# Optimization experiments

Hardware: AMD Instinct MI355X
Metric: run time of the kernel (lower is better)

Reference implementation:

```python
import jax, jax.numpy as jnp
import numpy as np

D_MODEL = 256   # per-head dim in this module
N_HEAD = 8
B, S = 4, 2048
NEG_INF = -1e9  # large negative in place of -inf for numerical safety


def setup_inputs() -> dict:
    key = jax.random.key(0)
    ks = jax.random.split(key, 8)
    d, h = D_MODEL, N_HEAD
    sc = 1.0 / np.sqrt(d)
    return {
        "Q": jax.random.normal(ks[0], (B, S, d), jnp.float32),
        "mask": jax.random.randint(ks[1], (B, S), 0, 2, jnp.int32),
        "WQ_w": jax.random.normal(ks[2], (h * d, d), jnp.float32) * sc,
        "WQ_b": jnp.zeros((h * d,), jnp.float32),
        "WK_w": jax.random.normal(ks[3], (h * d, d), jnp.float32) * sc,
        "WK_b": jnp.zeros((h * d,), jnp.float32),
        "WV_w": jax.random.normal(ks[4], (h * d, d), jnp.float32) * sc,
        "WV_b": jnp.zeros((h * d,), jnp.float32),
        "WO_w": jax.random.normal(ks[5], (d, h * d), jnp.float32) * sc,
        "WO_b": jnp.zeros((d,), jnp.float32),
        "ln_g": jnp.ones((d,), jnp.float32),
        "ln_b": jnp.zeros((d,), jnp.float32),
    }


def reference(Q, mask, WQ_w, WQ_b, WK_w, WK_b, WV_w, WV_b, WO_w, WO_b, ln_g, ln_b):
    b, s, d = Q.shape
    h = N_HEAD
    # projections (torch Linear: x @ W.T + b), split into heads: [b, h, s, d]
    q = (Q @ WQ_w.T + WQ_b).reshape(b, s, h, d).transpose(0, 2, 1, 3)
    k = (Q @ WK_w.T + WK_b).reshape(b, s, h, d).transpose(0, 2, 1, 3)
    v = (Q @ WV_w.T + WV_b).reshape(b, s, h, d).transpose(0, 2, 1, 3)
    # scaled dot-product scores [b, h, q, k]
    scores = jnp.einsum('bhqd,bhkd->bhqk', q, k) / jnp.sqrt(jnp.asarray(d, Q.dtype))
    key_mask = (mask != 0)[:, None, None, :]  # [b,1,1,k]
    scores = jnp.where(key_mask, scores, NEG_INF)
    alpha = jax.nn.softmax(scores, axis=-1)
    out = jnp.einsum('bhqk,bhkd->bhqd', alpha, v)
    out = out.transpose(0, 2, 1, 3).reshape(b, s, h * d)
    out = out @ WO_w.T + WO_b + Q  # dropout is identity in eval
    # LayerNorm over last dim
    mu = out.mean(-1, keepdims=True)
    var = out.var(-1, keepdims=True)
    return (out - mu) / jnp.sqrt(var + 1e-5) * ln_g + ln_b
```

## Files before the change

kernel.cpp:

```cpp
#include <hip/hip_runtime.h>
#include <cstddef>
#include <cstdint>

#define SQ 2048
#define DH 256
#define NH 8
#define BATCH 4
#define MROWS (BATCH*SQ)
#define HID (NH*DH)

typedef __attribute__((ext_vector_type(8)))  short bf16x8;
typedef __attribute__((ext_vector_type(16))) float f32x16;

typedef __attribute__((address_space(1))) const unsigned char gbuf_t;
typedef __attribute__((address_space(3))) unsigned char lbuf_t;

__device__ __forceinline__ void gl_lds16(const void* g, void* l) {
  __builtin_amdgcn_global_load_lds((gbuf_t*)g, (lbuf_t*)l, 16, 0, 0);
}

__device__ __forceinline__ unsigned short f2bf(float f) {
  unsigned u = __float_as_uint(f);
  unsigned r = (u + 0x7FFFu + ((u >> 16) & 1u)) >> 16;
  return (unsigned short)r;
}
__device__ __forceinline__ unsigned pk2(float a, float b) {
  return (unsigned)f2bf(a) | ((unsigned)f2bf(b) << 16);
}
__device__ __forceinline__ float fexp2(float x) {
  float r;
  asm("v_exp_f32 %0, %1" : "=v"(r) : "v"(x));
  return r;
}
__device__ __forceinline__ f32x16 zero16() {
  f32x16 v;
#pragma unroll
  for (int i = 0; i < 16; ++i) v[i] = 0.0f;
  return v;
}

__global__ void __launch_bounds__(256) cvt_kernel(
    const float* __restrict__ X,  const float* __restrict__ Wq,
    const float* __restrict__ Wk, const float* __restrict__ Wv,
    const float* __restrict__ Wo,
    unsigned short* __restrict__ Xb,  unsigned short* __restrict__ Wqb,
    unsigned short* __restrict__ Wkb, unsigned short* __restrict__ Wvb,
    unsigned short* __restrict__ Wob)
{
  int bid = blockIdx.x;
  const float* src; unsigned short* dst; size_t off;
  if      (bid < 512) { src = X;  dst = Xb;  off = (size_t)bid * 4096; }
  else if (bid < 640) { src = Wq; dst = Wqb; off = (size_t)(bid - 512) * 4096; }
  else if (bid < 768) { src = Wk; dst = Wkb; off = (size_t)(bid - 640) * 4096; }
  else if (bid < 896) { src = Wv; dst = Wvb; off = (size_t)(bid - 768) * 4096; }
  else                { src = Wo; dst = Wob; off = (size_t)(bid - 896) * 4096; }
  int tid = threadIdx.x;
#pragma unroll
  for (int k = 0; k < 4; ++k) {
    size_t idx = off + ((size_t)k * 256 + tid) * 4;
    float4 v = *(const float4*)(src + idx);
    uint2 o; o.x = pk2(v.x, v.y); o.y = pk2(v.z, v.w);
    *(uint2*)(dst + idx) = o;
  }
}

__global__ void __launch_bounds__(256) qkv_kernel(
    const unsigned short* __restrict__ Xbf,
    const unsigned short* __restrict__ Wqb,
    const unsigned short* __restrict__ Wkb,
    const unsigned short* __restrict__ Wvb,
    const float* __restrict__ bq, const float* __restrict__ bk, const float* __restrict__ bv,
    unsigned short* __restrict__ q_ws, unsigned short* __restrict__ k_ws,
    unsigned short* __restrict__ vt_ws)
{
  __shared__ unsigned char TA[65536];
  __shared__ unsigned char TB[65536];
  const int tid = threadIdx.x, w = tid >> 6, l = tid & 63;
  const int h = l >> 5, t = l & 31;
  const int wm = w >> 1, wn = w & 1;
  const int z = blockIdx.z;
  const int m0 = (z == 2) ? blockIdx.y * 128 : blockIdx.x * 128;
  const int n0 = (z == 2) ? blockIdx.x * 128 : blockIdx.y * 128;
  const unsigned short* Asrc = (z == 2) ? Wvb : Xbf;
  const unsigned short* Bsrc = (z == 0) ? Wqb : (z == 1) ? Wkb : Xbf;

  const int rowo = l >> 5;
  const int bin  = (l & 31) * 16;
#pragma unroll
  for (int i2 = 0; i2 < 16; ++i2) {
    int i = 16 * w + i2;
    int row = 2 * i + rowo;
    gl_lds16((const unsigned char*)(Asrc + (size_t)(m0 + row) * 256) + (bin ^ ((row & 15) << 4)),
             &TA[i * 1024]);
  }
#pragma unroll
  for (int i2 = 0; i2 < 16; ++i2) {
    int i = 16 * w + i2;
    int row = 2 * i + rowo;
    gl_lds16((const unsigned char*)(Bsrc + (size_t)(n0 + row) * 256) + (bin ^ ((row & 15) << 4)),
             &TB[i * 1024]);
  }
  __syncthreads();

  f32x16 acc00 = zero16(), acc01 = zero16(), acc10 = zero16(), acc11 = zero16();
  const int swz = (t & 15) << 4;
#pragma unroll
  for (int kc = 0; kc < 16; ++kc) {
    int kb = (32 * kc + 16 * h) ^ swz;
    bf16x8 a0 = *(const bf16x8*)&TA[(size_t)(64 * wm + t) * 512 + kb];
    bf16x8 a1 = *(const bf16x8*)&TA[(size_t)(64 * wm + 32 + t) * 512 + kb];
    bf16x8 b0 = *(const bf16x8*)&TB[(size_t)(64 * wn + t) * 512 + kb];
    bf16x8 b1 = *(const bf16x8*)&TB[(size_t)(64 * wn + 32 + t) * 512 + kb];
    acc00 = __builtin_amdgcn_mfma_f32_32x32x16_bf16(a0, b0, acc00, 0, 0, 0);
    acc01 = __builtin_amdgcn_mfma_f32_32x32x16_bf16(a0, b1, acc01, 0, 0, 0);
    acc10 = __builtin_amdgcn_mfma_f32_32x32x16_bf16(a1, b0, acc10, 0, 0, 0);
    acc11 = __builtin_amdgcn_mfma_f32_32x32x16_bf16(a1, b1, acc11, 0, 0, 0);
  }

  if (z < 2) {
    unsigned short* outp = z ? k_ws : q_ws;
    const float* bias = z ? bk : bq;
    float bn0 = bias[n0 + 64 * wn + t];
    float bn1 = bias[n0 + 64 * wn + 32 + t];
#pragma unroll
    for (int mt = 0; mt < 2; ++mt) {
#pragma unroll
      for (int nt = 0; nt < 2; ++nt) {
        int n = n0 + 64 * wn + 32 * nt + t;
        int headn = n >> 8, d = n & 255;
        float bb = nt ? bn1 : bn0;
        const f32x16& A = (mt == 0) ? (nt == 0 ? acc00 : acc01) : (nt == 0 ? acc10 : acc11);
#pragma unroll
        for (int r = 0; r < 16; ++r) {
          int m = m0 + 64 * wm + 32 * mt + (r & 3) + 8 * (r >> 2) + 4 * h;
          int batch = m >> 11, s = m & 2047;
          outp[(((size_t)batch * NH + headn) * SQ + s) * DH + d] = f2bf(A[r] + bb);
        }
      }
    }
  } else {
#pragma unroll
    for (int mt = 0; mt < 2; ++mt) {
#pragma unroll
      for (int r = 0; r < 16; ++r) {
        int j = m0 + 64 * wm + 32 * mt + (r & 3) + 8 * (r >> 2) + 4 * h;
        float bj = bv[j];
        int headj = j >> 8, jl = j & 255;
#pragma unroll
        for (int nt = 0; nt < 2; ++nt) {
          int sall = n0 + 64 * wn + 32 * nt + t;
          int batch = sall >> 11, ss = sall & 2047;
          const f32x16& A = (mt == 0) ? (nt == 0 ? acc00 : acc01) : (nt == 0 ? acc10 : acc11);
          vt_ws[((size_t)batch * NH + headj) * DH * SQ + (size_t)jl * SQ + ss] = f2bf(A[r] + bj);
        }
      }
    }
  }
}

__global__ void __launch_bounds__(512, 2) attn_kernel(
    const unsigned short* __restrict__ q_ws,
    const unsigned short* __restrict__ k_ws,
    const unsigned short* __restrict__ vt_ws,
    const int* __restrict__ mask,
    unsigned short* __restrict__ o_ws)
{
  __shared__ unsigned char KT[2][32768];
  __shared__ unsigned char VT[2][32768];
  __shared__ float MB[2048];

  const int tid = threadIdx.x, w = tid >> 6, l = tid & 63;
  const int h = l >> 5, t = l & 31;
  const int bid = blockIdx.x;
  const int xcd = bid & 7, slot = bid >> 3;
  const int bh = xcd * 4 + (slot >> 3);
  const int qt = slot & 7;
  const int b = bh >> 3, head = bh & 7;
  const int q0 = qt * 256;

  const float SC2 = 0.0625f * 1.44269504f;
  const float THR = 11.54f;

  {
    const int* mrow = mask + b * SQ;
    for (int i = tid; i < SQ; i += 512) MB[i] = mrow[i] ? 0.0f : -1.0e9f;
  }

  const unsigned short* kplane = k_ws + (size_t)bh * SQ * DH;
  const unsigned short* vplane = vt_ws + (size_t)bh * DH * SQ;

  bf16x8 qf[16];
  {
    const unsigned short* qb = q_ws + ((size_t)bh * SQ + (q0 + 32 * w + t)) * DH + 8 * h;
#pragma unroll
    for (int kc = 0; kc < 16; ++kc) qf[kc] = *(const bf16x8*)(qb + 16 * kc);
  }

  const int krow_o = l >> 5, kcol = (l & 31) * 16;
  const int vrow_o = l >> 3, vcol = (l & 7) * 16;

  {
#pragma unroll
    for (int i = 0; i < 4; ++i) {
      int j = 4 * w + i;
      int row = 2 * j + krow_o;
      gl_lds16((const unsigned char*)(kplane + (size_t)row * DH) + (kcol ^ ((row & 15) << 4)),
               &KT[0][j * 1024]);
    }
#pragma unroll
    for (int i = 0; i < 4; ++i) {
      int j = 4 * w + i;
      int row = 8 * j + vrow_o;
      gl_lds16((const unsigned char*)(vplane + (size_t)row * SQ) + (vcol ^ ((row & 7) << 4)),
               &VT[0][j * 1024]);
    }
  }
  __syncthreads();

  f32x16 o[8];
#pragma unroll
  for (int i = 0; i < 8; ++i) o[i] = zero16();
  float m_run = -3.0e38f, l_run = 0.0f;

  const int swzK = (t & 15) << 4;
  const int swzV = (t & 7) << 4;

  int cur = 0;
  for (int kb = 0; kb < SQ; kb += 64) {
    const int nxt = cur ^ 1;
    if (kb + 64 < SQ) {
#pragma unroll
      for (int i = 0; i < 4; ++i) {
        int j = 4 * w + i;
        int row = 2 * j + krow_o;
        gl_lds16((const unsigned char*)(kplane + (size_t)(kb + 64 + row) * DH) + (kcol ^ ((row & 15) << 4)),
                 &KT[nxt][j * 1024]);
      }
#pragma unroll
      for (int i = 0; i < 4; ++i) {
        int j = 4 * w + i;
        int row = 8 * j + vrow_o;
        gl_lds16((const unsigned char*)(vplane + (size_t)row * SQ + kb + 64) + (vcol ^ ((row & 7) << 4)),
                 &VT[nxt][j * 1024]);
      }
    }

    f32x16 sa0 = zero16(), sa1 = zero16();
    __builtin_amdgcn_s_setprio(1);
#pragma unroll
    for (int kc = 0; kc < 16; ++kc) {
      int kbb = (32 * kc + 16 * h) ^ swzK;
      bf16x8 a0 = *(const bf16x8*)&KT[cur][(size_t)t * 512 + kbb];
      bf16x8 a1 = *(const bf16x8*)&KT[cur][(size_t)(32 + t) * 512 + kbb];
      sa0 = __builtin_amdgcn_mfma_f32_32x32x16_bf16(a0, qf[kc], sa0, 0, 0, 0);
      sa1 = __builtin_amdgcn_mfma_f32_32x32x16_bf16(a1, qf[kc], sa1, 0, 0, 0);
    }
    __builtin_amdgcn_s_setprio(0);

#pragma unroll
    for (int g = 0; g < 4; ++g) {
      float4 m0v = *(const float4*)&MB[kb + 4 * h + 8 * g];
      float4 m1v = *(const float4*)&MB[kb + 32 + 4 * h + 8 * g];
      sa0[4*g+0] = sa0[4*g+0] * SC2 + m0v.x;
      sa0[4*g+1] = sa0[4*g+1] * SC2 + m0v.y;
      sa0[4*g+2] = sa0[4*g+2] * SC2 + m0v.z;
      sa0[4*g+3] = sa0[4*g+3] * SC2 + m0v.w;
      sa1[4*g+0] = sa1[4*g+0] * SC2 + m1v.x;
      sa1[4*g+1] = sa1[4*g+1] * SC2 + m1v.y;
      sa1[4*g+2] = sa1[4*g+2] * SC2 + m1v.z;
      sa1[4*g+3] = sa1[4*g+3] * SC2 + m1v.w;
    }
    f32x16 mm;
#pragma unroll
    for (int r = 0; r < 16; ++r) mm[r] = fmaxf(sa0[r], sa1[r]);
#pragma unroll
    for (int s = 8; s >= 1; s >>= 1) {
#pragma unroll
      for (int r = 0; r < 8; ++r) {
        if (r < s) mm[r] = fmaxf(mm[r], mm[r + s]);
      }
    }
    float tm = fmaxf(mm[0], __shfl_xor(mm[0], 32, 64));

    if (__builtin_expect(!__all(tm <= m_run + THR), 0)) {
      float m_new = fmaxf(m_run, tm);
      float rf = fexp2(m_run - m_new);
      m_run = m_new;
      l_run *= rf;
#pragma unroll
      for (int r = 0; r < 16; ++r) {
        float rr = __shfl(rf, (r & 3) + 8 * (r >> 2) + 4 * h, 64);
#pragma unroll
        for (int db = 0; db < 8; ++db) o[db][r] *= rr;
      }
    }

    float ssum = 0.0f;
#pragma unroll
    for (int ks = 0; ks < 4; ++ks) {
      const f32x16& P = (ks < 2) ? sa0 : sa1;
      const int base = 8 * (ks & 1);
      float e0 = fexp2(P[base + 0] - m_run);
      float e1 = fexp2(P[base + 1] - m_run);
      float e2 = fexp2(P[base + 2] - m_run);
      float e3 = fexp2(P[base + 3] - m_run);
      float e4 = fexp2(P[base + 4] - m_run);
      float e5 = fexp2(P[base + 5] - m_run);
      float e6 = fexp2(P[base + 6] - m_run);
      float e7 = fexp2(P[base + 7] - m_run);
      unsigned lo0, lo1, hi0, hi1;
      asm("v_cvt_pk_bf16_f32 %0, %1, %2" : "=v"(lo0) : "v"(e0), "v"(e1));
      asm("v_cvt_pk_bf16_f32 %0, %1, %2" : "=v"(lo1) : "v"(e2), "v"(e3));
      asm("v_cvt_pk_bf16_f32 %0, %1, %2" : "=v"(hi0) : "v"(e4), "v"(e5));
      asm("v_cvt_pk_bf16_f32 %0, %1, %2" : "=v"(hi1) : "v"(e6), "v"(e7));
      unsigned s0 = h ? lo0 : hi0;
      unsigned s1 = h ? lo1 : hi1;
      unsigned x0 = (unsigned)__shfl_xor((int)s0, 32, 64);
      unsigned x1 = (unsigned)__shfl_xor((int)s1, 32, 64);
      union { unsigned u[4]; bf16x8 v; } pu;
      pu.u[0] = h ? x0 : lo0;
      pu.u[1] = h ? x1 : lo1;
      pu.u[2] = h ? hi0 : x0;
      pu.u[3] = h ? hi1 : x1;
      bf16x8 pav = pu.v;
      ssum += ((e0 + e1) + (e2 + e3)) + ((e4 + e5) + (e6 + e7));
      __builtin_amdgcn_s_setprio(1);
#pragma unroll
      for (int db = 0; db < 8; ++db) {
        bf16x8 bv = *(const bf16x8*)&VT[cur][(size_t)(32 * db + t) * 128 + ((32 * ks + 16 * h) ^ swzV)];
        o[db] = __builtin_amdgcn_mfma_f32_32x32x16_bf16(pav, bv, o[db], 0, 0, 0);
      }
      __builtin_amdgcn_s_setprio(0);
    }
    float ls = ssum + __shfl_xor(ssum, 32, 64);
    l_run += ls;

    __syncthreads();
    cur = nxt;
  }

  float linv = 1.0f / l_run;
  unsigned short* ob = o_ws + (size_t)b * SQ * HID + (size_t)head * DH;
#pragma unroll
  for (int r = 0; r < 16; ++r) {
    int rowr = (r & 3) + 8 * (r >> 2) + 4 * h;
    float li = __shfl(linv, rowr, 64);
    int s = q0 + 32 * w + rowr;
    unsigned short* orow = ob + (size_t)s * HID;
#pragma unroll
    for (int db = 0; db < 8; ++db)
      orow[32 * db + t] = f2bf(o[db][r] * li);
  }
}

__global__ void __launch_bounds__(256) oproj_ln_kernel(
    const unsigned short* __restrict__ Abf,
    const unsigned short* __restrict__ Wob,
    const float* __restrict__ bo, const float* __restrict__ Xin,
    const float* __restrict__ g, const float* __restrict__ be,
    float* __restrict__ out)
{
  __shared__ unsigned char TA[4096];
  __shared__ unsigned char TB[32768];
  __shared__ float RS1[4][32], RS2[4][32];
  const int tid = threadIdx.x, w = tid >> 6, l = tid & 63;
  const int h = l >> 5, t = l & 31;
  const int m0 = blockIdx.x * 32;
  const int arow_o = l >> 3, ab_in = (l & 7) * 16;
  const int swz = (t & 7) << 4;

  f32x16 acc0 = zero16(), acc1 = zero16();
  for (int chunk = 0; chunk < 32; ++chunk) {
    __syncthreads();
    {
      int row = 8 * w + arow_o;
      gl_lds16((const unsigned char*)(Abf + (size_t)(m0 + row) * HID + chunk * 64) + (ab_in ^ ((row & 7) << 4)),
               &TA[w * 1024]);
    }
#pragma unroll
    for (int i2 = 0; i2 < 8; ++i2) {
      int j = 8 * w + i2;
      int row = 8 * j + arow_o;
      gl_lds16((const unsigned char*)(Wob + (size_t)row * HID + chunk * 64) + (ab_in ^ ((row & 7) << 4)),
               &TB[j * 1024]);
    }
    __syncthreads();
#pragma unroll
    for (int kc = 0; kc < 4; ++kc) {
      int kbb = (32 * kc + 16 * h) ^ swz;
      bf16x8 a  = *(const bf16x8*)&TA[(size_t)t * 128 + kbb];
      bf16x8 b0 = *(const bf16x8*)&TB[(size_t)(64 * w + t) * 128 + kbb];
      bf16x8 b1 = *(const bf16x8*)&TB[(size_t)(64 * w + 32 + t) * 128 + kbb];
      acc0 = __builtin_amdgcn_mfma_f32_32x32x16_bf16(a, b0, acc0, 0, 0, 0);
      acc1 = __builtin_amdgcn_mfma_f32_32x32x16_bf16(a, b1, acc1, 0, 0, 0);
    }
  }

  const int c0 = 64 * w + t, c1 = 64 * w + 32 + t;
  float bb0 = bo[c0], bb1 = bo[c1];
  float gc0 = g[c0],  gc1 = g[c1];
  float bc0 = be[c0], bc1 = be[c1];
#pragma unroll
  for (int r = 0; r < 16; ++r) {
    int row = m0 + (r & 3) + 8 * (r >> 2) + 4 * h;
    acc0[r] += bb0 + Xin[(size_t)row * DH + c0];
    acc1[r] += bb1 + Xin[(size_t)row * DH + c1];
  }

#pragma unroll
  for (int r = 0; r < 16; ++r) {
    float p1 = acc0[r] + acc1[r];
    float p2 = acc0[r] * acc0[r] + acc1[r] * acc1[r];
#pragma unroll
    for (int off = 1; off < 32; off <<= 1) {
      p1 += __shfl_xor(p1, off, 64);
      p2 += __shfl_xor(p2, off, 64);
    }
    if (t == 0) {
      int rl = (r & 3) + 8 * (r >> 2) + 4 * h;
      RS1[w][rl] = p1; RS2[w][rl] = p2;
    }
  }
  __syncthreads();

#pragma unroll
  for (int r = 0; r < 16; ++r) {
    int rl = (r & 3) + 8 * (r >> 2) + 4 * h;
    float s1 = (RS1[0][rl] + RS1[1][rl]) + (RS1[2][rl] + RS1[3][rl]);
    float s2 = (RS2[0][rl] + RS2[1][rl]) + (RS2[2][rl] + RS2[3][rl]);
    float mean = s1 * (1.0f / 256.0f);
    float var  = s2 * (1.0f / 256.0f) - mean * mean;
    float rstd = rsqrtf(var + 1e-5f);
    size_t rowo = (size_t)(m0 + rl) * DH;
    out[rowo + c0] = (acc0[r] - mean) * rstd * gc0 + bc0;
    out[rowo + c1] = (acc1[r] - mean) * rstd * gc1 + bc1;
  }
}

extern "C" void kernel_launch(void* const* d_in, const int* in_sizes, int n_in,
                              void* d_out, int out_size, void* d_ws, size_t ws_size,
                              hipStream_t stream) {
  const float* Q    = (const float*)d_in[0];
  const int*   mask = (const int*)  d_in[1];
  const float* WQ_w = (const float*)d_in[2];
  const float* WQ_b = (const float*)d_in[3];
  const float* WK_w = (const float*)d_in[4];
  const float* WK_b = (const float*)d_in[5];
  const float* WV_w = (const float*)d_in[6];
  const float* WV_b = (const float*)d_in[7];
  const float* WO_w = (const float*)d_in[8];
  const float* WO_b = (const float*)d_in[9];
  const float* ln_g = (const float*)d_in[10];
  const float* ln_b = (const float*)d_in[11];
  float* out = (float*)d_out;

  uint8_t* ws = (uint8_t*)d_ws;
  const size_t MB1 = 1048576;
  unsigned short* Xb   = (unsigned short*)(ws + 0 * MB1);
  unsigned short* Wqb  = (unsigned short*)(ws + 4 * MB1);
  unsigned short* Wkb  = (unsigned short*)(ws + 5 * MB1);
  unsigned short* Wvb  = (unsigned short*)(ws + 6 * MB1);
  unsigned short* Wob  = (unsigned short*)(ws + 7 * MB1);
  unsigned short* q_ws = (unsigned short*)(ws + 8 * MB1);
  unsigned short* k_ws = (unsigned short*)(ws + 40 * MB1);
  unsigned short* vtws = (unsigned short*)(ws + 72 * MB1);
  unsigned short* o_ws = (unsigned short*)(ws + 104 * MB1);

  cvt_kernel<<<1024, 256, 0, stream>>>(Q, WQ_w, WK_w, WV_w, WO_w, Xb, Wqb, Wkb, Wvb, Wob);
  qkv_kernel<<<dim3(64, 16, 3), 256, 0, stream>>>(Xb, Wqb, Wkb, Wvb, WQ_b, WK_b, WV_b,
                                                  q_ws, k_ws, vtws);
  attn_kernel<<<dim3(256), 512, 0, stream>>>(q_ws, k_ws, vtws, mask, o_ws);
  oproj_ln_kernel<<<dim3(256), 256, 0, stream>>>(o_ws, Wob, WO_b, Q, ln_g, ln_b, out);
}
```

Baseline: 297.2 us.

## Halve QKV LDS tiles for two-block occupancy and double-buffer O-proj loads

The QKV GEMM now stages K in two 128-wide chunks with 32KB A/B tiles instead of loading the full 256-wide K at once. This halves LDS use so two blocks can co-reside, with launch bounds raised to match. The output-projection kernel gets double-buffered LDS tiles so the next K chunk's global-to-LDS loads overlap the current chunk's MFMAs. In exchange, QKV gains an extra sync round, and the O-proj kernel's LDS footprint roughly doubles.

```diff
diff --git a/kernel.cpp b/kernel.cpp
--- a/kernel.cpp
+++ b/kernel.cpp
@@ -64,7 +64,7 @@
   }
 }
 
-__global__ void __launch_bounds__(256) qkv_kernel(
+__global__ void __launch_bounds__(256, 2) qkv_kernel(
     const unsigned short* __restrict__ Xbf,
     const unsigned short* __restrict__ Wqb,
     const unsigned short* __restrict__ Wkb,
@@ -73,8 +73,8 @@
     unsigned short* __restrict__ q_ws, unsigned short* __restrict__ k_ws,
     unsigned short* __restrict__ vt_ws)
 {
-  __shared__ unsigned char TA[65536];
-  __shared__ unsigned char TB[65536];
+  __shared__ unsigned char TA[32768];
+  __shared__ unsigned char TB[32768];
   const int tid = threadIdx.x, w = tid >> 6, l = tid & 63;
   const int h = l >> 5, t = l & 31;
   const int wm = w >> 1, wn = w & 1;
@@ -84,37 +84,43 @@
   const unsigned short* Asrc = (z == 2) ? Wvb : Xbf;
   const unsigned short* Bsrc = (z == 0) ? Wqb : (z == 1) ? Wkb : Xbf;
 
-  const int rowo = l >> 5;
-  const int bin  = (l & 31) * 16;
-#pragma unroll
-  for (int i2 = 0; i2 < 16; ++i2) {
-    int i = 16 * w + i2;
-    int row = 2 * i + rowo;
-    gl_lds16((const unsigned char*)(Asrc + (size_t)(m0 + row) * 256) + (bin ^ ((row & 15) << 4)),
-             &TA[i * 1024]);
-  }
-#pragma unroll
-  for (int i2 = 0; i2 < 16; ++i2) {
-    int i = 16 * w + i2;
-    int row = 2 * i + rowo;
-    gl_lds16((const unsigned char*)(Bsrc + (size_t)(n0 + row) * 256) + (bin ^ ((row & 15) << 4)),
-             &TB[i * 1024]);
-  }
-  __syncthreads();
+  const int rowo = l >> 4;
+  const int bin  = (l & 15) * 16;
+  const int swz  = (t & 15) << 4;
 
   f32x16 acc00 = zero16(), acc01 = zero16(), acc10 = zero16(), acc11 = zero16();
-  const int swz = (t & 15) << 4;
-#pragma unroll
-  for (int kc = 0; kc < 16; ++kc) {
-    int kb = (32 * kc + 16 * h) ^ swz;
-    bf16x8 a0 = *(const bf16x8*)&TA[(size_t)(64 * wm + t) * 512 + kb];
-    bf16x8 a1 = *(const bf16x8*)&TA[(size_t)(64 * wm + 32 + t) * 512 + kb];
-    bf16x8 b0 = *(const bf16x8*)&TB[(size_t)(64 * wn + t) * 512 + kb];
-    bf16x8 b1 = *(const bf16x8*)&TB[(size_t)(64 * wn + 32 + t) * 512 + kb];
-    acc00 = __builtin_amdgcn_mfma_f32_32x32x16_bf16(a0, b0, acc00, 0, 0, 0);
-    acc01 = __builtin_amdgcn_mfma_f32_32x32x16_bf16(a0, b1, acc01, 0, 0, 0);
-    acc10 = __builtin_amdgcn_mfma_f32_32x32x16_bf16(a1, b0, acc10, 0, 0, 0);
-    acc11 = __builtin_amdgcn_mfma_f32_32x32x16_bf16(a1, b1, acc11, 0, 0, 0);
+
+  for (int chunk = 0; chunk < 2; ++chunk) {
+    __syncthreads();
+#pragma unroll
+    for (int i2 = 0; i2 < 8; ++i2) {
+      int j = 8 * w + i2;
+      int row = 4 * j + rowo;
+      gl_lds16((const unsigned char*)(Asrc + (size_t)(m0 + row) * 256 + chunk * 128)
+                 + (bin ^ ((row & 15) << 4)),
+               &TA[j * 1024]);
+    }
+#pragma unroll
+    for (int i2 = 0; i2 < 8; ++i2) {
+      int j = 8 * w + i2;
+      int row = 4 * j + rowo;
+      gl_lds16((const unsigned char*)(Bsrc + (size_t)(n0 + row) * 256 + chunk * 128)
+                 + (bin ^ ((row & 15) << 4)),
+               &TB[j * 1024]);
+    }
+    __syncthreads();
+#pragma unroll
+    for (int kc = 0; kc < 8; ++kc) {
+      int kb = (32 * kc + 16 * h) ^ swz;
+      bf16x8 a0 = *(const bf16x8*)&TA[(size_t)(64 * wm + t) * 256 + kb];
+      bf16x8 a1 = *(const bf16x8*)&TA[(size_t)(64 * wm + 32 + t) * 256 + kb];
+      bf16x8 b0 = *(const bf16x8*)&TB[(size_t)(64 * wn + t) * 256 + kb];
+      bf16x8 b1 = *(const bf16x8*)&TB[(size_t)(64 * wn + 32 + t) * 256 + kb];
+      acc00 = __builtin_amdgcn_mfma_f32_32x32x16_bf16(a0, b0, acc00, 0, 0, 0);
+      acc01 = __builtin_amdgcn_mfma_f32_32x32x16_bf16(a0, b1, acc01, 0, 0, 0);
+      acc10 = __builtin_amdgcn_mfma_f32_32x32x16_bf16(a1, b0, acc10, 0, 0, 0);
+      acc11 = __builtin_amdgcn_mfma_f32_32x32x16_bf16(a1, b1, acc11, 0, 0, 0);
+    }
   }
 
   if (z < 2) {
@@ -353,15 +359,15 @@
   }
 }
 
-__global__ void __launch_bounds__(256) oproj_ln_kernel(
+__global__ void __launch_bounds__(256, 2) oproj_ln_kernel(
     const unsigned short* __restrict__ Abf,
     const unsigned short* __restrict__ Wob,
     const float* __restrict__ bo, const float* __restrict__ Xin,
     const float* __restrict__ g, const float* __restrict__ be,
     float* __restrict__ out)
 {
-  __shared__ unsigned char TA[4096];
-  __shared__ unsigned char TB[32768];
+  __shared__ unsigned char TA[2][4096];
+  __shared__ unsigned char TB[2][32768];
   __shared__ float RS1[4][32], RS2[4][32];
   const int tid = threadIdx.x, w = tid >> 6, l = tid & 63;
   const int h = l >> 5, t = l & 31;
@@ -369,31 +375,47 @@
   const int arow_o = l >> 3, ab_in = (l & 7) * 16;
   const int swz = (t & 7) << 4;
 
-  f32x16 acc0 = zero16(), acc1 = zero16();
-  for (int chunk = 0; chunk < 32; ++chunk) {
-    __syncthreads();
-    {
-      int row = 8 * w + arow_o;
-      gl_lds16((const unsigned char*)(Abf + (size_t)(m0 + row) * HID + chunk * 64) + (ab_in ^ ((row & 7) << 4)),
-               &TA[w * 1024]);
-    }
+  {
+    int row = 8 * w + arow_o;
+    gl_lds16((const unsigned char*)(Abf + (size_t)(m0 + row) * HID) + (ab_in ^ ((row & 7) << 4)),
+             &TA[0][w * 1024]);
 #pragma unroll
     for (int i2 = 0; i2 < 8; ++i2) {
       int j = 8 * w + i2;
-      int row = 8 * j + arow_o;
-      gl_lds16((const unsigned char*)(Wob + (size_t)row * HID + chunk * 64) + (ab_in ^ ((row & 7) << 4)),
-               &TB[j * 1024]);
-    }
-    __syncthreads();
+      int row2 = 8 * j + arow_o;
+      gl_lds16((const unsigned char*)(Wob + (size_t)row2 * HID) + (ab_in ^ ((row2 & 7) << 4)),
+               &TB[0][j * 1024]);
+    }
+  }
+  __syncthreads();
+
+  f32x16 acc0 = zero16(), acc1 = zero16();
+  int cur = 0;
+  for (int chunk = 0; chunk < 32; ++chunk) {
+    const int nxt = cur ^ 1;
+    if (chunk + 1 < 32) {
+      int row = 8 * w + arow_o;
+      gl_lds16((const unsigned char*)(Abf + (size_t)(m0 + row) * HID + (chunk + 1) * 64) + (ab_in ^ ((row & 7) << 4)),
+               &TA[nxt][w * 1024]);
+#pragma unroll
+      for (int i2 = 0; i2 < 8; ++i2) {
+        int j = 8 * w + i2;
+        int row2 = 8 * j + arow_o;
+        gl_lds16((const unsigned char*)(Wob + (size_t)row2 * HID + (chunk + 1) * 64) + (ab_in ^ ((row2 & 7) << 4)),
+                 &TB[nxt][j * 1024]);
+      }
+    }
 #pragma unroll
     for (int kc = 0; kc < 4; ++kc) {
       int kbb = (32 * kc + 16 * h) ^ swz;
-      bf16x8 a  = *(const bf16x8*)&TA[(size_t)t * 128 + kbb];
-      bf16x8 b0 = *(const bf16x8*)&TB[(size_t)(64 * w + t) * 128 + kbb];
-      bf16x8 b1 = *(const bf16x8*)&TB[(size_t)(64 * w + 32 + t) * 128 + kbb];
+      bf16x8 a  = *(const bf16x8*)&TA[cur][(size_t)t * 128 + kbb];
+      bf16x8 b0 = *(const bf16x8*)&TB[cur][(size_t)(64 * w + t) * 128 + kbb];
+      bf16x8 b1 = *(const bf16x8*)&TB[cur][(size_t)(64 * w + 32 + t) * 128 + kbb];
       acc0 = __builtin_amdgcn_mfma_f32_32x32x16_bf16(a, b0, acc0, 0, 0, 0);
       acc1 = __builtin_amdgcn_mfma_f32_32x32x16_bf16(a, b1, acc1, 0, 0, 0);
     }
+    __syncthreads();
+    cur = nxt;
   }
 
   const int c0 = 64 * w + t, c1 = 64 * w + 32 + t;
```

New measurement: 283.8 us, median of 2. 4.5% less time.
